# Performance work log

Measured on AMD Instinct MI355X. Metric: run time of the kernel, lower is better.

## Reference

```python
import jax, jax.numpy as jnp
import numpy as np

NHEAD = 16


def setup_inputs() -> dict:
    key = jax.random.key(0)
    ks = jax.random.split(key, 8)
    B, T, C = 2, 1024, 2048
    H, D = NHEAD, C // NHEAD
    P = 1024  # past kv length
    s = 0.02
    return {
        "x": jax.random.normal(ks[0], (B, T, C), jnp.float32),
        "past_k": jax.random.normal(ks[1], (B, H, P, D), jnp.float32),
        "past_v": jax.random.normal(ks[2], (B, H, P, D), jnp.float32),
        "Wk": jax.random.normal(ks[3], (C, C), jnp.float32) * s,
        "Wq": jax.random.normal(ks[4], (C, C), jnp.float32) * s,
        "Wv": jax.random.normal(ks[5], (C, C), jnp.float32) * s,
        "Wp": jax.random.normal(ks[6], (C, C), jnp.float32) * s,
        "bp": jax.random.normal(ks[7], (C,), jnp.float32) * s,
    }


def reference(x, past_k, past_v, Wk, Wq, Wv, Wp, bp):
    B, T, C = x.shape
    H = NHEAD
    D = C // H
    # nn.Linear(W): y = x @ W.T ; split into heads -> [B,H,T,D]
    def proj_heads(W):
        return (x @ W.T).reshape(B, T, H, D).transpose(0, 2, 1, 3)
    q = proj_heads(Wq)
    k_new = proj_heads(Wk)
    v_new = proj_heads(Wv)
    k = jnp.concatenate([past_k, k_new], axis=2)  # [B,H,P+T,D]
    v = jnp.concatenate([past_v, v_new], axis=2)
    past_len = past_k.shape[2]
    total_len = past_len + T
    # causal mask: new-query row i attends to absolute position j <= past_len + i
    q_pos = past_len + jnp.arange(T)[:, None]        # [T,1]
    k_pos = jnp.arange(total_len)[None, :]           # [1,total]
    mask = k_pos <= q_pos                            # [T,total]
    att = jnp.einsum("bhqd,bhkd->bhqk", q, k) * (1.0 / np.sqrt(D).astype(np.float32))
    att = jnp.where(mask[None, None], att, jnp.float32(-jnp.inf))
    att = jax.nn.softmax(att, axis=-1)
    out = jnp.einsum("bhqk,bhkd->bhqd", att, v)
    out = out.transpose(0, 2, 1, 3).reshape(B, T, C)
    out = out @ Wp.T + bp
    return out, k, v
```

## Files before the change

kernel.cpp:

```cpp
#include <hip/hip_runtime.h>
#include <stdint.h>

#define B_ 2
#define T_ 1024
#define C_ 2048
#define H_ 16
#define D_ 128
#define P_ 1024
#define L_ 2048
#define M_ 2048

typedef unsigned short u16;
typedef __attribute__((ext_vector_type(8))) short short8;
typedef __attribute__((ext_vector_type(4))) float f32x4;
typedef __attribute__((ext_vector_type(8))) u16 u16x8;
typedef __attribute__((ext_vector_type(4))) u16 u16x4;

__device__ __forceinline__ u16 f2bf(float x) {
    union { float f; uint32_t u; } c; c.f = x;
    uint32_t u = c.u;
    return (u16)((u + 0x7fffu + ((u >> 16) & 1u)) >> 16);
}

__device__ __forceinline__ void gload_lds16(const void* g, void* l) {
    typedef __attribute__((address_space(1))) const void gvoid;
    typedef __attribute__((address_space(3))) void lvoid;
    __builtin_amdgcn_global_load_lds((gvoid*)g, (lvoid*)l, 16, 0, 0);
}

__global__ __launch_bounds__(256) void prep_kernel(
        const float* __restrict__ x,  const float* __restrict__ wk,
        const float* __restrict__ wv, const float* __restrict__ wq,
        const float4* __restrict__ pk, const float4* __restrict__ pv,
        u16* __restrict__ xb, u16* __restrict__ obK,
        u16* __restrict__ obV, u16* __restrict__ obQ,
        float4* __restrict__ kdst, float4* __restrict__ vdst,
        u16x4* __restrict__ kb, u16* __restrict__ vbT) {
    __shared__ float s[64][65];
    const int bid = blockIdx.x;
    const int tid = threadIdx.x;
    if (bid < 8192) {
        const int r = bid >> 11;
        const int i = (bid & 2047) * 256 + tid;
        const float* src = (r == 0) ? x : (r == 1) ? wk : (r == 2) ? wv : wq;
        u16* dst = (r == 0) ? xb : (r == 1) ? obK : (r == 2) ? obV : obQ;
        float4 a = ((const float4*)src)[i * 2], b = ((const float4*)src)[i * 2 + 1];
        ((u16x8*)dst)[i] = u16x8{f2bf(a.x), f2bf(a.y), f2bf(a.z), f2bf(a.w),
                                 f2bf(b.x), f2bf(b.y), f2bf(b.z), f2bf(b.w)};
    } else if (bid < 12288) {
        const int i = (bid - 8192) * 256 + tid;
        const int bh = i >> 15;
        const int rest = i & 32767;
        const size_t dst = (size_t)bh * (L_ * D_ / 4) + rest;
        float4 k4 = pk[i], v4 = pv[i];
        kdst[dst] = k4;
        vdst[dst] = v4;
        kb[dst] = u16x4{f2bf(k4.x), f2bf(k4.y), f2bf(k4.z), f2bf(k4.w)};
    } else {
        const int tb = bid - 12288;
        const int bh = tb >> 5;
        const int tile = tb & 31;
        const int k0 = (tile >> 1) * 64;
        const int d0 = (tile & 1) * 64;
        const float* src = (const float*)pv + ((size_t)bh * P_ + k0) * D_ + d0;
        {
            int r = tid >> 2, c0 = (tid & 3) * 16;
#pragma unroll
            for (int u = 0; u < 4; ++u) {
                float4 f = *(const float4*)(src + (size_t)r * D_ + c0 + u * 4);
                s[r][c0 + u * 4 + 0] = f.x; s[r][c0 + u * 4 + 1] = f.y;
                s[r][c0 + u * 4 + 2] = f.z; s[r][c0 + u * 4 + 3] = f.w;
            }
        }
        __syncthreads();
        int d = tid >> 2, ck = (tid & 3) * 16;
        u16* dst = vbT + ((size_t)bh * D_ + d0 + d) * L_ + k0 + ck;
        u16x8 o0, o1;
#pragma unroll
        for (int j = 0; j < 8; ++j) o0[j] = f2bf(s[ck + j][d]);
#pragma unroll
        for (int j = 0; j < 8; ++j) o1[j] = f2bf(s[ck + 8 + j][d]);
        *(u16x8*)dst = o0;
        *(u16x8*)(dst + 8) = o1;
    }
}

__global__ __launch_bounds__(256) void convert_bf16_kernel(
        const float* __restrict__ in, u16* __restrict__ out) {
    int i = blockIdx.x * 256 + threadIdx.x;
    const float4* p = (const float4*)in;
    float4 a = p[i * 2], b = p[i * 2 + 1];
    ((u16x8*)out)[i] = u16x8{f2bf(a.x), f2bf(a.y), f2bf(a.z), f2bf(a.w),
                             f2bf(b.x), f2bf(b.y), f2bf(b.z), f2bf(b.w)};
}

__global__ __launch_bounds__(256) void gemm_qkv(
        const u16* __restrict__ A,
        const u16* __restrict__ wbK, const u16* __restrict__ wbV,
        const u16* __restrict__ wbQ,
        float* __restrict__ kout, float* __restrict__ vout,
        u16* __restrict__ kb, u16* __restrict__ vbT, u16* __restrict__ Qst) {
    __shared__ u16 As[2][128 * 32];
    __shared__ u16 Bs[2][128 * 32];
    const int tid  = threadIdx.x;
    const int wave = tid >> 6;
    const int lane = tid & 63;
    const int m0   = blockIdx.y * 128;
    const int n0g  = blockIdx.x * 128;
    const int region = n0g >> 11;
    const int n0   = n0g & 2047;
    const u16* Bw = (region == 0) ? wbK : (region == 1) ? wbV : wbQ;

    f32x4 acc[4][4];
#pragma unroll
    for (int i = 0; i < 4; ++i)
#pragma unroll
        for (int j = 0; j < 4; ++j) acc[i][j] = f32x4{0.f, 0.f, 0.f, 0.f};

    const int srow = lane >> 2;
    const int scol = (lane & 3) * 8;
    const int q0 = wave * 2, q1 = wave * 2 + 1;
    const u16* A0 = A  + (size_t)(m0 + q0 * 16 + srow) * C_ + scol;
    const u16* A1 = A  + (size_t)(m0 + q1 * 16 + srow) * C_ + scol;
    const u16* B0 = Bw + (size_t)(n0 + q0 * 16 + srow) * C_ + scol;
    const u16* B1 = Bw + (size_t)(n0 + q1 * 16 + srow) * C_ + scol;

    const int frow = lane & 15;
    const int fko  = (lane >> 4) * 8;
    const int wr = (wave >> 1) * 64;
    const int wc = (wave & 1) * 64;

    gload_lds16(A0, &As[0][q0 * 512]);
    gload_lds16(A1, &As[0][q1 * 512]);
    gload_lds16(B0, &Bs[0][q0 * 512]);
    gload_lds16(B1, &Bs[0][q1 * 512]);
    __syncthreads();

    int cur = 0;
    for (int kt = 0; kt < C_; kt += 32) {
        const int nxt = cur ^ 1;
        if (kt + 32 < C_) {
            gload_lds16(A0 + kt + 32, &As[nxt][q0 * 512]);
            gload_lds16(A1 + kt + 32, &As[nxt][q1 * 512]);
            gload_lds16(B0 + kt + 32, &Bs[nxt][q0 * 512]);
            gload_lds16(B1 + kt + 32, &Bs[nxt][q1 * 512]);
        }
        short8 af[4], bf[4];
#pragma unroll
        for (int i = 0; i < 4; ++i) {
            af[i] = *(const short8*)&As[cur][(wr + i * 16 + frow) * 32 + fko];
            bf[i] = *(const short8*)&Bs[cur][(wc + i * 16 + frow) * 32 + fko];
        }
#pragma unroll
        for (int mi = 0; mi < 4; ++mi)
#pragma unroll
            for (int ni = 0; ni < 4; ++ni)
                acc[mi][ni] = __builtin_amdgcn_mfma_f32_16x16x32_bf16(
                    af[mi], bf[ni], acc[mi][ni], 0, 0, 0);
        __syncthreads();
        cur = nxt;
    }

    const int ccol = lane & 15;
    const int crb  = (lane >> 4) * 4;
#pragma unroll
    for (int mi = 0; mi < 4; ++mi) {
#pragma unroll
        for (int ni = 0; ni < 4; ++ni) {
            const int gc  = n0 + wc + ni * 16 + ccol;
            const int grb = m0 + wr + mi * 16 + crb;
            if (region == 2) {
#pragma unroll
                for (int r = 0; r < 4; ++r)
                    Qst[(size_t)(grb + r) * C_ + gc] = f2bf(acc[mi][ni][r]);
            } else {
                const int b = grb >> 10, tb = grb & 1023;
                const int h = gc >> 7,  d  = gc & 127;
                const size_t fb = (((size_t)(b * H_ + h)) * L_ + P_ + tb) * D_ + d;
                if (region == 0) {
#pragma unroll
                    for (int r = 0; r < 4; ++r) {
                        kout[fb + (size_t)r * D_] = acc[mi][ni][r];
                        kb[fb + (size_t)r * D_]   = f2bf(acc[mi][ni][r]);
                    }
                } else {
#pragma unroll
                    for (int r = 0; r < 4; ++r) vout[fb + (size_t)r * D_] = acc[mi][ni][r];
                    const size_t tb2 = (((size_t)(b * H_ + h)) * D_ + d) * L_ + P_ + tb;
                    *(u16x4*)&vbT[tb2] = u16x4{
                        f2bf(acc[mi][ni][0]), f2bf(acc[mi][ni][1]),
                        f2bf(acc[mi][ni][2]), f2bf(acc[mi][ni][3])};
                }
            }
        }
    }
}

template <int MODE>
__global__ __launch_bounds__(256) void gemm128(
        const u16* __restrict__ A, const u16* __restrict__ Bw,
        float* __restrict__ outf, u16* __restrict__ outb,
        const float* __restrict__ bias) {
    __shared__ u16 As[2][128 * 32];
    __shared__ u16 Bs[2][128 * 32];
    const int tid  = threadIdx.x;
    const int wave = tid >> 6;
    const int lane = tid & 63;
    const int m0 = blockIdx.y * 128;
    const int n0 = blockIdx.x * 128;

    f32x4 acc[4][4];
#pragma unroll
    for (int i = 0; i < 4; ++i)
#pragma unroll
        for (int j = 0; j < 4; ++j) acc[i][j] = f32x4{0.f, 0.f, 0.f, 0.f};

    const int srow = lane >> 2;
    const int scol = (lane & 3) * 8;
    const int q0 = wave * 2, q1 = wave * 2 + 1;
    const u16* A0 = A  + (size_t)(m0 + q0 * 16 + srow) * C_ + scol;
    const u16* A1 = A  + (size_t)(m0 + q1 * 16 + srow) * C_ + scol;
    const u16* B0 = Bw + (size_t)(n0 + q0 * 16 + srow) * C_ + scol;
    const u16* B1 = Bw + (size_t)(n0 + q1 * 16 + srow) * C_ + scol;

    const int frow = lane & 15;
    const int fko  = (lane >> 4) * 8;
    const int wr = (wave >> 1) * 64;
    const int wc = (wave & 1) * 64;

    gload_lds16(A0, &As[0][q0 * 512]);
    gload_lds16(A1, &As[0][q1 * 512]);
    gload_lds16(B0, &Bs[0][q0 * 512]);
    gload_lds16(B1, &Bs[0][q1 * 512]);
    __syncthreads();

    int cur = 0;
    for (int kt = 0; kt < C_; kt += 32) {
        const int nxt = cur ^ 1;
        if (kt + 32 < C_) {
            gload_lds16(A0 + kt + 32, &As[nxt][q0 * 512]);
            gload_lds16(A1 + kt + 32, &As[nxt][q1 * 512]);
            gload_lds16(B0 + kt + 32, &Bs[nxt][q0 * 512]);
            gload_lds16(B1 + kt + 32, &Bs[nxt][q1 * 512]);
        }
        short8 af[4], bf[4];
#pragma unroll
        for (int i = 0; i < 4; ++i) {
            af[i] = *(const short8*)&As[cur][(wr + i * 16 + frow) * 32 + fko];
            bf[i] = *(const short8*)&Bs[cur][(wc + i * 16 + frow) * 32 + fko];
        }
#pragma unroll
        for (int mi = 0; mi < 4; ++mi)
#pragma unroll
            for (int ni = 0; ni < 4; ++ni)
                acc[mi][ni] = __builtin_amdgcn_mfma_f32_16x16x32_bf16(
                    af[mi], bf[ni], acc[mi][ni], 0, 0, 0);
        __syncthreads();
        cur = nxt;
    }

    const int ccol = lane & 15;
    const int crb  = (lane >> 4) * 4;
#pragma unroll
    for (int mi = 0; mi < 4; ++mi) {
#pragma unroll
        for (int ni = 0; ni < 4; ++ni) {
            const int gc  = n0 + wc + ni * 16 + ccol;
            const int grb = m0 + wr + mi * 16 + crb;
            if (MODE == 0) {
#pragma unroll
                for (int r = 0; r < 4; ++r)
                    outb[(size_t)(grb + r) * C_ + gc] = f2bf(acc[mi][ni][r]);
            } else {
                const float ba = bias[gc];
#pragma unroll
                for (int r = 0; r < 4; ++r)
                    outf[(size_t)(grb + r) * C_ + gc] = acc[mi][ni][r] + ba;
            }
        }
    }
}

#define NEG_BIG -30000.f
__global__ __launch_bounds__(256) void attn_kernel(
        const u16* __restrict__ Q, const u16* __restrict__ Kb,
        const u16* __restrict__ VT, u16* __restrict__ O) {
    __shared__ u16 Qs[64 * 128];
    __shared__ u16 Ks[64 * 128];
    __shared__ u16 Vs[128 * 64];
    __shared__ u16 Ps[64][72];

    const int tid  = threadIdx.x;
    const int wave = tid >> 6;
    const int lane = tid & 63;
    int       qt = blockIdx.x & 15;
    const int h  = (blockIdx.x >> 4) & 15;
    const int b  = blockIdx.x >> 8;
    if (b) qt = 15 - qt;
    const int t0 = qt * 64;

    const u16* Kbase = Kb + (size_t)(b * H_ + h) * L_ * D_;
    const u16* Vbase = VT + (size_t)(b * H_ + h) * D_ * L_;

#pragma unroll
    for (int i = 0; i < 4; ++i) {
        int g   = (wave * 4 + i) * 64 + lane;
        int row = g >> 4, blk = g & 15;
        int sb  = (blk & 8) | ((blk ^ row) & 7);
        gload_lds16(Q + ((size_t)(b * T_ + t0 + row)) * C_ + h * D_ + sb * 8,
                    &Qs[(wave * 4 + i) * 512]);
    }

    const int frow = lane & 15;
    const int quad = lane >> 4;
    const int fko  = quad * 8;
    const int swz  = (frow & 7) << 3;

    f32x4 o_acc[8];
#pragma unroll
    for (int n = 0; n < 8; ++n) o_acc[n] = f32x4{0.f, 0.f, 0.f, 0.f};
    float m_i[4] = {NEG_BIG, NEG_BIG, NEG_BIG, NEG_BIG};
    float l_i[4] = {0.f, 0.f, 0.f, 0.f};
    const float scale = 0.08838834764831845f;

    const int nch = (P_ + t0 + 64) >> 6;
    const int wave_lim = P_ + t0 + wave * 16 + 15;

    for (int ch = 0; ch < nch; ++ch) {
        const int j0 = ch * 64;
        __syncthreads();
#pragma unroll
        for (int i = 0; i < 4; ++i) {
            int g = (wave * 4 + i) * 64 + lane;
            {
                int row = g >> 4, blk = g & 15;
                int sb  = (blk & 8) | ((blk ^ row) & 7);
                gload_lds16(Kbase + (size_t)(j0 + row) * D_ + sb * 8,
                            &Ks[(wave * 4 + i) * 512]);
            }
            {
                int d  = g >> 3, cb = g & 7;
                int sb = (cb ^ d) & 7;
                gload_lds16(Vbase + (size_t)d * L_ + j0 + sb * 8,
                            &Vs[(wave * 4 + i) * 512]);
            }
        }
        __syncthreads();

        const bool active = (j0 <= wave_lim);

        if (active) {
            f32x4 st[4];
#pragma unroll
            for (int j = 0; j < 4; ++j) st[j] = f32x4{0.f, 0.f, 0.f, 0.f};
            __builtin_amdgcn_s_setprio(1);
#pragma unroll
            for (int kt = 0; kt < 4; ++kt) {
                short8 a = *(const short8*)&Qs[(wave * 16 + frow) * 128 +
                                               ((kt * 32 + fko) ^ swz)];
#pragma unroll
                for (int j = 0; j < 4; ++j) {
                    short8 kf = *(const short8*)&Ks[(j * 16 + frow) * 128 +
                                                    ((kt * 32 + fko) ^ swz)];
                    st[j] = __builtin_amdgcn_mfma_f32_16x16x32_bf16(a, kf, st[j], 0, 0, 0);
                }
            }
            __builtin_amdgcn_s_setprio(0);

#pragma unroll
            for (int r = 0; r < 4; ++r) {
                const int t   = t0 + wave * 16 + quad * 4 + r;
                const int lim = P_ + t;
                float sv[4];
                float mx = NEG_BIG;
#pragma unroll
                for (int j = 0; j < 4; ++j) {
                    int jg = j0 + j * 16 + frow;
                    float s = st[j][r] * scale;
                    s = (jg <= lim) ? s : NEG_BIG;
                    sv[j] = s;
                    mx = fmaxf(mx, s);
                }
#pragma unroll
                for (int sft = 1; sft <= 8; sft <<= 1)
                    mx = fmaxf(mx, __shfl_xor(mx, sft, 64));
                float m_new = fmaxf(m_i[r], mx);
                float alpha = __expf(fminf(m_i[r] - m_new, 0.f));
                float rs = 0.f;
#pragma unroll
                for (int j = 0; j < 4; ++j) {
                    float p = __expf(fminf(sv[j] - m_new, 0.f));
                    p = (sv[j] <= NEG_BIG) ? 0.f : p;
                    sv[j] = p;
                    rs += p;
                }
#pragma unroll
                for (int sft = 1; sft <= 8; sft <<= 1)
                    rs += __shfl_xor(rs, sft, 64);
                l_i[r] = l_i[r] * alpha + rs;
                m_i[r] = m_new;
#pragma unroll
                for (int n = 0; n < 8; ++n) o_acc[n][r] *= alpha;
#pragma unroll
                for (int j = 0; j < 4; ++j)
                    Ps[wave * 16 + quad * 4 + r][j * 16 + frow] = f2bf(sv[j]);
            }
        }
        __syncthreads();

        if (active) {
            __builtin_amdgcn_s_setprio(1);
#pragma unroll
            for (int kt2 = 0; kt2 < 2; ++kt2) {
                short8 a = *(const short8*)&Ps[wave * 16 + frow][kt2 * 32 + fko];
#pragma unroll
                for (int n = 0; n < 8; ++n) {
                    short8 vf = *(const short8*)&Vs[(n * 16 + frow) * 64 +
                                                    ((kt2 * 32 + fko) ^ swz)];
                    o_acc[n] = __builtin_amdgcn_mfma_f32_16x16x32_bf16(a, vf, o_acc[n], 0, 0, 0);
                }
            }
            __builtin_amdgcn_s_setprio(0);
        }
    }

#pragma unroll
    for (int r = 0; r < 4; ++r) {
        float rl = 1.f / fmaxf(l_i[r], 1e-30f);
        int t = t0 + wave * 16 + quad * 4 + r;
#pragma unroll
        for (int n = 0; n < 8; ++n) {
            float v = o_acc[n][r] * rl;
            O[((size_t)(b * T_ + t)) * C_ + h * D_ + n * 16 + frow] = f2bf(v);
        }
    }
}

extern "C" void kernel_launch(void* const* d_in, const int* in_sizes, int n_in,
                              void* d_out, int out_size, void* d_ws, size_t ws_size,
                              hipStream_t stream) {
    const float* x      = (const float*)d_in[0];
    const float* past_k = (const float*)d_in[1];
    const float* past_v = (const float*)d_in[2];
    const float* Wk     = (const float*)d_in[3];
    const float* Wq     = (const float*)d_in[4];
    const float* Wv     = (const float*)d_in[5];
    const float* Wp     = (const float*)d_in[6];
    const float* bp     = (const float*)d_in[7];

    float* out  = (float*)d_out;
    float* kout = out + 4194304;
    float* vout = kout + 8388608;

    u16* Qst = (u16*)d_out;
    u16* xb  = (u16*)((char*)d_out + (8u << 20));
    u16* OstWq = (u16*)d_ws;
    u16* kb    = (u16*)((char*)d_ws + (8u  << 20));
    u16* vbT   = (u16*)((char*)d_ws + (24u << 20));
    u16* wbKP  = (u16*)((char*)d_ws + (40u << 20));
    const bool fused = ws_size >= (size_t)(56u << 20);
    u16* wbV = fused ? (u16*)((char*)d_ws + (48u << 20))
                     : Qst;

    prep_kernel<<<13312, 256, 0, stream>>>(
        x, Wk, Wv, Wq,
        (const float4*)past_k, (const float4*)past_v,
        xb, wbKP, wbV, OstWq,
        (float4*)kout, (float4*)vout, (u16x4*)kb, vbT);

    if (fused) {
        dim3 g(48, 16);
        gemm_qkv<<<g, 256, 0, stream>>>(xb, wbKP, wbV, OstWq,
                                        kout, vout, kb, vbT, Qst);
    } else {
        dim3 gkv(32, 16);
        gemm_qkv<<<gkv, 256, 0, stream>>>(xb, wbKP, wbV, OstWq,
                                          kout, vout, kb, vbT, Qst);
        dim3 gq(16, 16);
        gemm128<0><<<gq, 256, 0, stream>>>(xb, OstWq, nullptr, Qst, nullptr);
    }

    attn_kernel<<<512, 256, 0, stream>>>(Qst, kb, vbT, OstWq);

    convert_bf16_kernel<<<2048, 256, 0, stream>>>(Wp, wbKP);
    dim3 gp(16, 16);
    gemm128<2><<<gp, 256, 0, stream>>>(OstWq, wbKP, out, nullptr, bp);
}
```

Measured before the change: 420.5 us.

## Triple-buffer GEMM LDS pipeline and fold Wp conversion into prep kernel

Both GEMM kernels move from double-buffered LDS with two barriers per k-step to a three-stage ring. Loads are issued two tiles ahead, and a partial vmcnt wait plus a single barrier per iteration lets global-to-LDS loads overlap more of the MFMA work. When the workspace holds at least 64MB, the Wp fp32-to-bf16 conversion moves into the prep kernel as extra blocks, which removes a separate launch. This costs 50% more LDS per block, which may lower occupancy, and the hand-written waitcnt sequencing could break if the compiler reorders the loads.

New measurement: 386.3 us. -8.1%, faster.

```diff
diff --git a/kernel.cpp b/kernel.cpp
--- a/kernel.cpp
+++ b/kernel.cpp
@@ -31,9 +31,10 @@
 __global__ __launch_bounds__(256) void prep_kernel(
         const float* __restrict__ x,  const float* __restrict__ wk,
         const float* __restrict__ wv, const float* __restrict__ wq,
+        const float* __restrict__ wp,
         const float4* __restrict__ pk, const float4* __restrict__ pv,
         u16* __restrict__ xb, u16* __restrict__ obK,
-        u16* __restrict__ obV, u16* __restrict__ obQ,
+        u16* __restrict__ obV, u16* __restrict__ obQ, u16* __restrict__ obP,
         float4* __restrict__ kdst, float4* __restrict__ vdst,
         u16x4* __restrict__ kb, u16* __restrict__ vbT) {
     __shared__ float s[64][65];
@@ -56,7 +57,7 @@
         kdst[dst] = k4;
         vdst[dst] = v4;
         kb[dst] = u16x4{f2bf(k4.x), f2bf(k4.y), f2bf(k4.z), f2bf(k4.w)};
-    } else {
+    } else if (bid < 13312) {
         const int tb = bid - 12288;
         const int bh = tb >> 5;
         const int tile = tb & 31;
@@ -82,6 +83,11 @@
         for (int j = 0; j < 8; ++j) o1[j] = f2bf(s[ck + 8 + j][d]);
         *(u16x8*)dst = o0;
         *(u16x8*)(dst + 8) = o1;
+    } else {
+        const int i = (bid - 13312) * 256 + tid;
+        float4 a = ((const float4*)wp)[i * 2], b = ((const float4*)wp)[i * 2 + 1];
+        ((u16x8*)obP)[i] = u16x8{f2bf(a.x), f2bf(a.y), f2bf(a.z), f2bf(a.w),
+                                 f2bf(b.x), f2bf(b.y), f2bf(b.z), f2bf(b.w)};
     }
 }
 
@@ -94,14 +100,15 @@
                              f2bf(b.x), f2bf(b.y), f2bf(b.z), f2bf(b.w)};
 }
 
+
 __global__ __launch_bounds__(256) void gemm_qkv(
         const u16* __restrict__ A,
         const u16* __restrict__ wbK, const u16* __restrict__ wbV,
         const u16* __restrict__ wbQ,
         float* __restrict__ kout, float* __restrict__ vout,
         u16* __restrict__ kb, u16* __restrict__ vbT, u16* __restrict__ Qst) {
-    __shared__ u16 As[2][128 * 32];
-    __shared__ u16 Bs[2][128 * 32];
+    __shared__ u16 As[3][128 * 32];
+    __shared__ u16 Bs[3][128 * 32];
     const int tid  = threadIdx.x;
     const int wave = tid >> 6;
     const int lane = tid & 63;
@@ -130,26 +137,33 @@
     const int wr = (wave >> 1) * 64;
     const int wc = (wave & 1) * 64;
 
-    gload_lds16(A0, &As[0][q0 * 512]);
-    gload_lds16(A1, &As[0][q1 * 512]);
-    gload_lds16(B0, &Bs[0][q0 * 512]);
-    gload_lds16(B1, &Bs[0][q1 * 512]);
-    __syncthreads();
-
-    int cur = 0;
-    for (int kt = 0; kt < C_; kt += 32) {
-        const int nxt = cur ^ 1;
-        if (kt + 32 < C_) {
-            gload_lds16(A0 + kt + 32, &As[nxt][q0 * 512]);
-            gload_lds16(A1 + kt + 32, &As[nxt][q1 * 512]);
-            gload_lds16(B0 + kt + 32, &Bs[nxt][q0 * 512]);
-            gload_lds16(B1 + kt + 32, &Bs[nxt][q1 * 512]);
+    u16 *Ac = &As[0][0], *An = &As[1][0], *Af = &As[2][0];
+    u16 *Bc = &Bs[0][0], *Bn = &Bs[1][0], *Bf = &Bs[2][0];
+
+    gload_lds16(A0,      Ac + q0 * 512);
+    gload_lds16(A1,      Ac + q1 * 512);
+    gload_lds16(B0,      Bc + q0 * 512);
+    gload_lds16(B1,      Bc + q1 * 512);
+    gload_lds16(A0 + 32, An + q0 * 512);
+    gload_lds16(A1 + 32, An + q1 * 512);
+    gload_lds16(B0 + 32, Bn + q0 * 512);
+    gload_lds16(B1 + 32, Bn + q1 * 512);
+
+    for (int kt = 0; kt < C_ - 32; kt += 32) {
+        asm volatile("s_waitcnt vmcnt(4)" ::: "memory");
+        __builtin_amdgcn_s_barrier();
+        asm volatile("" ::: "memory");
+        if (kt + 64 < C_) {
+            gload_lds16(A0 + kt + 64, Af + q0 * 512);
+            gload_lds16(A1 + kt + 64, Af + q1 * 512);
+            gload_lds16(B0 + kt + 64, Bf + q0 * 512);
+            gload_lds16(B1 + kt + 64, Bf + q1 * 512);
         }
         short8 af[4], bf[4];
 #pragma unroll
         for (int i = 0; i < 4; ++i) {
-            af[i] = *(const short8*)&As[cur][(wr + i * 16 + frow) * 32 + fko];
-            bf[i] = *(const short8*)&Bs[cur][(wc + i * 16 + frow) * 32 + fko];
+            af[i] = *(const short8*)&Ac[(wr + i * 16 + frow) * 32 + fko];
+            bf[i] = *(const short8*)&Bc[(wc + i * 16 + frow) * 32 + fko];
         }
 #pragma unroll
         for (int mi = 0; mi < 4; ++mi)
@@ -157,8 +171,26 @@
             for (int ni = 0; ni < 4; ++ni)
                 acc[mi][ni] = __builtin_amdgcn_mfma_f32_16x16x32_bf16(
                     af[mi], bf[ni], acc[mi][ni], 0, 0, 0);
-        __syncthreads();
-        cur = nxt;
+        u16* t;
+        t = Ac; Ac = An; An = Af; Af = t;
+        t = Bc; Bc = Bn; Bn = Bf; Bf = t;
+    }
+    {
+        asm volatile("s_waitcnt vmcnt(0)" ::: "memory");
+        __builtin_amdgcn_s_barrier();
+        asm volatile("" ::: "memory");
+        short8 af[4], bf[4];
+#pragma unroll
+        for (int i = 0; i < 4; ++i) {
+            af[i] = *(const short8*)&Ac[(wr + i * 16 + frow) * 32 + fko];
+            bf[i] = *(const short8*)&Bc[(wc + i * 16 + frow) * 32 + fko];
+        }
+#pragma unroll
+        for (int mi = 0; mi < 4; ++mi)
+#pragma unroll
+            for (int ni = 0; ni < 4; ++ni)
+                acc[mi][ni] = __builtin_amdgcn_mfma_f32_16x16x32_bf16(
+                    af[mi], bf[ni], acc[mi][ni], 0, 0, 0);
     }
 
     const int ccol = lane & 15;
@@ -201,8 +233,8 @@
         const u16* __restrict__ A, const u16* __restrict__ Bw,
         float* __restrict__ outf, u16* __restrict__ outb,
         const float* __restrict__ bias) {
-    __shared__ u16 As[2][128 * 32];
-    __shared__ u16 Bs[2][128 * 32];
+    __shared__ u16 As[3][128 * 32];
+    __shared__ u16 Bs[3][128 * 32];
     const int tid  = threadIdx.x;
     const int wave = tid >> 6;
     const int lane = tid & 63;
@@ -228,26 +260,33 @@
     const int wr = (wave >> 1) * 64;
     const int wc = (wave & 1) * 64;
 
-    gload_lds16(A0, &As[0][q0 * 512]);
-    gload_lds16(A1, &As[0][q1 * 512]);
-    gload_lds16(B0, &Bs[0][q0 * 512]);
-    gload_lds16(B1, &Bs[0][q1 * 512]);
-    __syncthreads();
-
-    int cur = 0;
-    for (int kt = 0; kt < C_; kt += 32) {
-        const int nxt = cur ^ 1;
-        if (kt + 32 < C_) {
-            gload_lds16(A0 + kt + 32, &As[nxt][q0 * 512]);
-            gload_lds16(A1 + kt + 32, &As[nxt][q1 * 512]);
-            gload_lds16(B0 + kt + 32, &Bs[nxt][q0 * 512]);
-            gload_lds16(B1 + kt + 32, &Bs[nxt][q1 * 512]);
+    u16 *Ac = &As[0][0], *An = &As[1][0], *Af = &As[2][0];
+    u16 *Bc = &Bs[0][0], *Bn = &Bs[1][0], *Bf = &Bs[2][0];
+
+    gload_lds16(A0,      Ac + q0 * 512);
+    gload_lds16(A1,      Ac + q1 * 512);
+    gload_lds16(B0,      Bc + q0 * 512);
+    gload_lds16(B1,      Bc + q1 * 512);
+    gload_lds16(A0 + 32, An + q0 * 512);
+    gload_lds16(A1 + 32, An + q1 * 512);
+    gload_lds16(B0 + 32, Bn + q0 * 512);
+    gload_lds16(B1 + 32, Bn + q1 * 512);
+
+    for (int kt = 0; kt < C_ - 32; kt += 32) {
+        asm volatile("s_waitcnt vmcnt(4)" ::: "memory");
+        __builtin_amdgcn_s_barrier();
+        asm volatile("" ::: "memory");
+        if (kt + 64 < C_) {
+            gload_lds16(A0 + kt + 64, Af + q0 * 512);
+            gload_lds16(A1 + kt + 64, Af + q1 * 512);
+            gload_lds16(B0 + kt + 64, Bf + q0 * 512);
+            gload_lds16(B1 + kt + 64, Bf + q1 * 512);
         }
         short8 af[4], bf[4];
 #pragma unroll
         for (int i = 0; i < 4; ++i) {
-            af[i] = *(const short8*)&As[cur][(wr + i * 16 + frow) * 32 + fko];
-            bf[i] = *(const short8*)&Bs[cur][(wc + i * 16 + frow) * 32 + fko];
+            af[i] = *(const short8*)&Ac[(wr + i * 16 + frow) * 32 + fko];
+            bf[i] = *(const short8*)&Bc[(wc + i * 16 + frow) * 32 + fko];
         }
 #pragma unroll
         for (int mi = 0; mi < 4; ++mi)
@@ -255,8 +294,26 @@
             for (int ni = 0; ni < 4; ++ni)
                 acc[mi][ni] = __builtin_amdgcn_mfma_f32_16x16x32_bf16(
                     af[mi], bf[ni], acc[mi][ni], 0, 0, 0);
-        __syncthreads();
-        cur = nxt;
+        u16* t;
+        t = Ac; Ac = An; An = Af; Af = t;
+        t = Bc; Bc = Bn; Bn = Bf; Bf = t;
+    }
+    {
+        asm volatile("s_waitcnt vmcnt(0)" ::: "memory");
+        __builtin_amdgcn_s_barrier();
+        asm volatile("" ::: "memory");
+        short8 af[4], bf[4];
+#pragma unroll
+        for (int i = 0; i < 4; ++i) {
+            af[i] = *(const short8*)&Ac[(wr + i * 16 + frow) * 32 + fko];
+            bf[i] = *(const short8*)&Bc[(wc + i * 16 + frow) * 32 + fko];
+        }
+#pragma unroll
+        for (int mi = 0; mi < 4; ++mi)
+#pragma unroll
+            for (int ni = 0; ni < 4; ++ni)
+                acc[mi][ni] = __builtin_amdgcn_mfma_f32_16x16x32_bf16(
+                    af[mi], bf[ni], acc[mi][ni], 0, 0, 0);
     }
 
     const int ccol = lane & 15;
@@ -459,13 +516,15 @@
     u16* vbT   = (u16*)((char*)d_ws + (24u << 20));
     u16* wbKP  = (u16*)((char*)d_ws + (40u << 20));
     const bool fused = ws_size >= (size_t)(56u << 20);
+    const bool bigws = ws_size >= (size_t)(64u << 20);
     u16* wbV = fused ? (u16*)((char*)d_ws + (48u << 20))
                      : Qst;
-
-    prep_kernel<<<13312, 256, 0, stream>>>(
-        x, Wk, Wv, Wq,
+    u16* wbP = bigws ? (u16*)((char*)d_ws + (56u << 20)) : wbKP;
+
+    prep_kernel<<<bigws ? 15360 : 13312, 256, 0, stream>>>(
+        x, Wk, Wv, Wq, Wp,
         (const float4*)past_k, (const float4*)past_v,
-        xb, wbKP, wbV, OstWq,
+        xb, wbKP, wbV, OstWq, bigws ? wbP : nullptr,
         (float4*)kout, (float4*)vout, (u16x4*)kb, vbT);
 
     if (fused) {
@@ -482,7 +541,7 @@
 
     attn_kernel<<<512, 256, 0, stream>>>(Qst, kb, vbT, OstWq);
 
-    convert_bf16_kernel<<<2048, 256, 0, stream>>>(Wp, wbKP);
+    if (!bigws) convert_bf16_kernel<<<2048, 256, 0, stream>>>(Wp, wbKP);
     dim3 gp(16, 16);
-    gemm128<2><<<gp, 256, 0, stream>>>(OstWq, wbKP, out, nullptr, bp);
-}
+    gemm128<2><<<gp, 256, 0, stream>>>(OstWq, wbP, out, nullptr, bp);
+}
```
